# Performance work log

Measured on AMD Instinct MI355X. Metric: run time of the kernel, lower is better.

Reference implementation:

```python
import jax, jax.numpy as jnp
import numpy as np

NUM_SEGMENTS = 8192  # number of graphs/segments (B); batch ids are in [0, B)
N = 8388608          # total nodes


def setup_inputs() -> dict:
    key = jax.random.key(0)
    k1, k2 = jax.random.split(key)
    x = jax.random.normal(k1, (N,), dtype=jnp.float32)
    batch = jnp.sort(jax.random.randint(k2, (N,), 0, NUM_SEGMENTS))
    return {"x": x, "batch": batch}


def _sparsemax(x, batch):
    n = x.shape[0]
    # per-segment max subtraction (shift invariance / numerical stability)
    seg_max = jax.ops.segment_max(x, batch, num_segments=NUM_SEGMENTS)
    xs = x - seg_max[batch]

    # segmented descending sort: primary key = batch, secondary = -x
    order = jnp.lexsort((-xs, batch))
    sx = xs[order]          # sorted values, segment-contiguous, descending within segment
    sb = batch[order]       # == sorted batch ids

    # segment sizes and start offsets
    num_nodes = jax.ops.segment_sum(jnp.ones_like(batch), batch, num_segments=NUM_SEGMENTS)
    cum = jnp.concatenate([jnp.zeros((1,), num_nodes.dtype), jnp.cumsum(num_nodes)[:-1]])

    # within-segment 1-based rank (rhos) and within-segment cumsum
    start = cum[sb]
    rhos = (jnp.arange(n) - start + 1).astype(x.dtype)
    c = jnp.cumsum(sx)
    base = jnp.where(start > 0, c[jnp.maximum(start - 1, 0)], jnp.zeros((), x.dtype))
    seg_cumsum = c - base

    # sparsemax support: rho * z_sorted > cumsum - 1
    support = rhos * sx > seg_cumsum - 1.0
    supp_size = jax.ops.segment_sum(support.astype(num_nodes.dtype), sb, num_segments=NUM_SEGMENTS)

    # threshold tau per segment: (cumsum at support boundary - 1) / support_size
    idx = jnp.clip(cum + supp_size - 1, 0, n - 1)
    tau = (seg_cumsum[idx] - 1.0) / jnp.maximum(supp_size, 1).astype(x.dtype)

    return jnp.maximum(xs - tau[batch], 0.0)


def reference(x, batch):
    return _sparsemax(x, batch)
```

## Files before the change

### kernel.cpp

```cpp
#include <hip/hip_runtime.h>


#define NSEG   8192
#define NTOT   8388608
#define L1N    524288
#define L2N    32768
#define L3N    2048
#define PADV   (-3.0e38f)
#define WREG   1216
#define FBB    256

__device__ __forceinline__ int esw(const int e) {
    return (e & ~15) | ((e + (e >> 4)) & 15);
}

__device__ __forceinline__ void cs(float& a, float& b, const bool up) {
    const float lo = fminf(a, b), hi = fmaxf(a, b);
    a = up ? hi : lo;
    b = up ? lo : hi;
}

__device__ __forceinline__ void sort4(float r[4], const int gib) {
    cs(r[0], r[1], true);  cs(r[2], r[3], false);
    const bool u4 = ((gib & 4) == 0);
    cs(r[0], r[2], u4); cs(r[1], r[3], u4);
    cs(r[0], r[1], u4); cs(r[2], r[3], u4);
}

template<int K>
__device__ __forceinline__ void bmerge4(float r[4], const int gib) {
    const bool up = ((gib & K) == 0);
    #pragma unroll
    for (int j = K >> 1; j >= 4; j >>= 1) {
        const bool tkm = (up == ((gib & j) == 0));
        const int tm = j >> 2;
        #pragma unroll
        for (int m = 0; m < 4; ++m) {
            const float p = __shfl_xor(r[m], tm, 64);
            r[m] = tkm ? fmaxf(r[m], p) : fminf(r[m], p);
        }
    }
    #pragma unroll
    for (int j = 2; j >= 1; j >>= 1)
        #pragma unroll
        for (int m = 0; m < 4; ++m)
            if ((m & j) == 0) cs(r[m], r[m | j], up);
}

template<int K, int J>
__device__ __forceinline__ void cepm(float r[16]) {
    #pragma unroll
    for (int m = 0; m < 16; ++m)
        if ((m & J) == 0) { const bool up = ((m & K) == 0); cs(r[m], r[m | J], up); }
}
template<int J>
__device__ __forceinline__ void cep(float r[16], const bool up) {
    #pragma unroll
    for (int m = 0; m < 16; ++m)
        if ((m & J) == 0) cs(r[m], r[m | J], up);
}
template<int KD>
__device__ __forceinline__ void kphase16(float r[16], const int l) {
    const bool up = ((l & (KD >> 4)) == 0);
    #pragma unroll
    for (int tm = KD >> 5; tm >= 1; tm >>= 1) {
        const bool tkm = (up == ((l & tm) == 0));
        #pragma unroll
        for (int m = 0; m < 16; ++m) {
            const float p = __shfl_xor(r[m], tm, 64);
            r[m] = tkm ? fmaxf(r[m], p) : fminf(r[m], p);
        }
    }
    cep<8>(r, up); cep<4>(r, up); cep<2>(r, up); cep<1>(r, up);
}
__device__ __forceinline__ void wsort1024(float r[16], const int l) {
    cepm<2, 1>(r);
    cepm<4, 2>(r); cepm<4, 1>(r);
    cepm<8, 4>(r); cepm<8, 2>(r); cepm<8, 1>(r);
    kphase16<16>(r, l);  kphase16<32>(r, l);  kphase16<64>(r, l);
    kphase16<128>(r, l); kphase16<256>(r, l); kphase16<512>(r, l);
    kphase16<1024>(r, l);
}

__global__ __launch_bounds__(256) void k1_bounds(
    const int* __restrict__ batch, int* __restrict__ starts, const int n)
{
    const int i = blockIdx.x * blockDim.x + threadIdx.x;
    if (i >= n) return;
    const int bi = batch[i];
    int bp = __shfl_up(bi, 1, 64);
    if (((threadIdx.x & 63) == 0) && i > 0) bp = batch[i - 1];
    if (i == 0) { for (int b = 0; b <= bi; ++b) starts[b] = 0; }
    else {
        for (int b = bp + 1; b <= bi; ++b) starts[b] = i;
    }
    if (i == n - 1) { for (int b = bi + 1; b <= NSEG; ++b) starts[b] = n; }
}

__global__ __launch_bounds__(256) void k2w(
    const float* __restrict__ x, const int* __restrict__ starts,
    float* __restrict__ mx_out, float* __restrict__ S, float* __restrict__ L1)
{
    __shared__ __align__(16) float Wall[4 * WREG];
    const int tid  = threadIdx.x;
    const int lane = tid & 63;
    const int wid  = tid >> 6;
    float* W = Wall + wid * WREG;

    const int b = blockIdx.x * 4 + wid;
    const int s = starts[b], e = starts[b + 1];
    const int n = e - s;
    if (n <= 0) { if (lane == 0) mx_out[b] = 0.0f; return; }

    const bool med = (n > 1024);
    const int  nb  = n - 1024;

    float r[16], rb[4];
    #pragma unroll
    for (int m = 0; m < 16; ++m) { const int i = 16 * lane + m; r[m] = (i < n) ? x[s + i] : PADV; }
    if (med) {
        #pragma unroll
        for (int m = 0; m < 4; ++m) { const int i = 1024 + 4 * lane + m; rb[m] = (i < n) ? x[s + i] : PADV; }
    }

    float mx = r[0];
    #pragma unroll
    for (int m = 1; m < 16; ++m) mx = fmaxf(mx, r[m]);
    if (med) {
        #pragma unroll
        for (int m = 0; m < 4; ++m) mx = fmaxf(mx, rb[m]);
    }
    #pragma unroll
    for (int o = 32; o; o >>= 1) mx = fmaxf(mx, __shfl_xor(mx, o, 64));
    if (lane == 0) mx_out[b] = mx;

    #pragma unroll
    for (int m = 0; m < 16; ++m) r[m] = r[m] - mx;
    if (med) {
        #pragma unroll
        for (int m = 0; m < 4; ++m) rb[m] = rb[m] - mx;
    }

    wsort1024(r, lane);

    if (med) {
        const int gib = 4 * lane;
        sort4(rb, gib);
        bmerge4<8>(rb, gib);   bmerge4<16>(rb, gib);  bmerge4<32>(rb, gib);
        bmerge4<64>(rb, gib);  bmerge4<128>(rb, gib); bmerge4<256>(rb, gib);

        #pragma unroll
        for (int m = 0; m < 16; ++m) W[esw(16 * lane + m)] = r[m];
        #pragma unroll
        for (int m = 0; m < 4; ++m) {
            const int i4 = 4 * lane + m;
            if (i4 < nb) W[esw(1024 + i4)] = rb[m];
        }

        float mg[20];
        const int d0 = 20 * lane;
        int cnt = 0;
        if (d0 < n) {
            int lo = (d0 > nb) ? d0 - nb : 0;
            int hi = (d0 < 1024) ? d0 : 1024;
            while (lo < hi) {
                const int a = (lo + hi) >> 1;
                if (W[esw(a)] >= W[esw(1024 + d0 - a - 1)]) lo = a + 1; else hi = a;
            }
            int i = lo, j = d0 - lo;
            cnt = (d0 + 20 < n) ? 20 : (n - d0);
            if (cnt > 20) cnt = 20;
            float va = (i < 1024) ? W[esw(i)] : 0.0f;
            float vb = (j < nb)   ? W[esw(1024 + j)] : 0.0f;
            #pragma unroll
            for (int kk = 0; kk < 20; ++kk) {
                if (kk < cnt) {
                    const bool tA = (j >= nb) || (i < 1024 && va >= vb);
                    if (tA) { mg[kk] = va; ++i; va = (i < 1024) ? W[esw(i)] : 0.0f; }
                    else    { mg[kk] = vb; ++j; vb = (j < nb)   ? W[esw(1024 + j)] : 0.0f; }
                }
            }
        }
        for (int kk = 0; kk < cnt; ++kk) W[esw(d0 + kk)] = mg[kk];
    } else {
        #pragma unroll
        for (int m = 0; m < 16; ++m) W[esw(16 * lane + m)] = r[m];
    }

    for (int i = lane; i < n; i += 64) S[s + i] = W[esw(i)];

    const int q0 = (s + 15) >> 4, q1 = e >> 4;
    for (int rr = lane; rr < q1 - q0; rr += 64) {
        const int lb = ((q0 + rr) << 4) - s;
        float v[16];
        #pragma unroll
        for (int ii = 0; ii < 16; ++ii) v[ii] = W[esw(lb + ii)];
        float a = 0.0f;
        #pragma unroll
        for (int ii = 0; ii < 16; ++ii) a = a + v[ii];
        L1[q0 + rr] = a;
    }
}

__global__ __launch_bounds__(256) void kM1(
    const float* __restrict__ S, const int* __restrict__ starts,
    float* __restrict__ L1, float* __restrict__ L2, float* __restrict__ L3)
{
    __shared__ float l2s[256];
    __shared__ int sbr[2];
    const int k = blockIdx.x, tid = threadIdx.x;

    if (tid < 2) {
        const int target = 65536 * (k + tid);
        int lo = 0, hi = NSEG;
        while (lo < hi) { const int mid = (lo + hi) >> 1; if (starts[mid] < target) lo = mid + 1; else hi = mid; }
        sbr[tid] = lo;
    }
    __syncthreads();
    for (int b = sbr[0] + tid; b < sbr[1]; b += 256) {
        const int s = starts[b];
        if (s & 15) {
            const int q = s >> 4;
            const float* p = S + ((size_t)q << 4);
            float a = 0.0f;
            #pragma unroll
            for (int i = 0; i < 16; ++i) a = a + p[i];
            L1[q] = a;
        }
    }
    __syncthreads();

    const int q2 = (k << 8) + tid;
    {
        const float* p = L1 + ((size_t)q2 << 4);
        float a = 0.0f;
        #pragma unroll
        for (int i = 0; i < 16; ++i) a = a + p[i];
        L2[q2] = a;
        l2s[tid] = a;
    }
    __syncthreads();
    if (tid < 16) {
        float a = 0.0f;
        #pragma unroll
        for (int i = 0; i < 16; ++i) a = a + l2s[(tid << 4) + i];
        L3[(k << 4) + tid] = a;
    }
}

__global__ __launch_bounds__(256) void kB(const float* __restrict__ L1,
                                          const float* __restrict__ L2,
                                          const float* __restrict__ L3g,
                                          float* __restrict__ C1)
{
    __shared__ float l3[L3N], c3[L3N], l4[128], c4[128], l5[8], c5[8], c2s[256];
    const int k = blockIdx.x, tid = threadIdx.x;

    for (int q = tid; q < L3N; q += 256) l3[q] = L3g[q];
    __syncthreads();
    if (tid < 128) {
        float a = 0.0f;
        for (int i = 0; i < 16; ++i) a = a + l3[tid * 16 + i];
        l4[tid] = a;
    }
    __syncthreads();
    if (tid < 8) {
        float a = 0.0f;
        for (int i = 0; i < 16; ++i) a = a + l4[tid * 16 + i];
        l5[tid] = a;
    }
    __syncthreads();
    if (tid == 0) {
        float a = 0.0f;
        for (int i = 0; i < 8; ++i) { a = a + l5[i]; c5[i] = a; }
    }
    __syncthreads();
    if (tid < 8) {
        const float pre = tid ? c5[tid - 1] : 0.0f;
        float a = 0.0f;
        for (int i = 0; i < 16; ++i) { a = a + l4[tid * 16 + i]; c4[tid * 16 + i] = tid ? (a + pre) : a; }
    }
    __syncthreads();
    if (tid < 128) {
        const float pre = tid ? c4[tid - 1] : 0.0f;
        float a = 0.0f;
        for (int i = 0; i < 16; ++i) { a = a + l3[tid * 16 + i]; c3[tid * 16 + i] = tid ? (a + pre) : a; }
    }
    __syncthreads();
    if (tid < 16) {
        const int q2r = (k << 4) + tid;
        const float pre = q2r ? c3[q2r - 1] : 0.0f;
        const float* p = L2 + ((size_t)q2r << 4);
        float a = 0.0f;
        #pragma unroll
        for (int i = 0; i < 16; ++i) { a = a + p[i]; c2s[(tid << 4) + i] = q2r ? (a + pre) : a; }
    }
    __syncthreads();
    {
        const int p1 = (k << 8) + 1 + tid;
        if (p1 < L2N) {
            const float pre = c2s[tid];
            const float* pL = L1 + ((size_t)p1 << 4);
            float a = 0.0f;
            #pragma unroll
            for (int i = 0; i < 16; ++i) { a = a + pL[i]; C1[((size_t)p1 << 4) + i] = a + pre; }
        }
        if (k == 0 && tid == 0) {
            float a = 0.0f;
            #pragma unroll
            for (int i = 0; i < 16; ++i) { a = a + L1[i]; C1[i] = a; }
        }
    }
}

__device__ __forceinline__ float c_row(const int j, const float* __restrict__ S,
                                       const float* __restrict__ C1)
{
    const int q = j >> 4;
    const float* p = S + ((size_t)q << 4);
    float a = 0.0f;
    for (int i = 0; i <= (j & 15); ++i) a = a + p[i];
    return q ? (a + C1[q - 1]) : a;
}

__global__ __launch_bounds__(128) void kCF(
    const float* __restrict__ x, const float* __restrict__ S, const float* __restrict__ C1,
    const int* __restrict__ starts, const int* __restrict__ batch,
    const float* __restrict__ mx, float* __restrict__ out)
{
    __shared__ float stau[1], sbase[1];
    __shared__ int   scnt[2];

    const int b = blockIdx.x, tid = threadIdx.x;
    const int s = starts[b], e = starts[b + 1];
    const int n = e - s;
    if (n <= 0) return;

    if (tid == 0) sbase[0] = (s > 0) ? c_row(s - 1, S, C1) : 0.0f;
    __syncthreads();
    const float base = sbase[0];

    const int q0 = s >> 4;
    const int nrows = ((e - 1) >> 4) - q0 + 1;
    const int R = (nrows < 32) ? nrows : 32;

    int cnt = 0;
    for (int rr = tid; rr < R; rr += 128) {
        const int q = q0 + rr;
        const float pre = q ? C1[q - 1] : 0.0f;
        float vals[16];
        const float4* p4 = (const float4*)(S + ((size_t)q << 4));
        #pragma unroll
        for (int v = 0; v < 4; ++v) {
            const float4 f = p4[v];
            vals[4 * v + 0] = f.x; vals[4 * v + 1] = f.y;
            vals[4 * v + 2] = f.z; vals[4 * v + 3] = f.w;
        }
        float a = 0.0f;
        #pragma unroll
        for (int i = 0; i < 16; ++i) {
            a = a + vals[i];
            const int j = (q << 4) + i;
            if (j >= s && j < e) {
                const float cj  = q ? (a + pre) : a;
                const float seg = (cj - base) - 1.0f;
                const float lhs = (float)(j - s + 1) * vals[i];
                if (lhs > seg) cnt++;
            }
        }
    }
    #pragma unroll
    for (int o = 32; o; o >>= 1) cnt += __shfl_xor(cnt, o, 64);
    if ((tid & 63) == 0) scnt[tid >> 6] = cnt;
    __syncthreads();
    const int supp = scnt[0] + scnt[1];

    if (tid == 0) {
        float t;
        if (supp > 0) {
            const int idx = s + supp - 1;
            const float ci = c_row(idx, S, C1);
            t = ((ci - base) - 1.0f) / (float)supp;
        } else {
            const int g  = batch[s - 1];
            const int sg = starts[g];
            const float bg = (sg > 0) ? c_row(sg - 1, S, C1) : 0.0f;
            t = (base - bg) - 1.0f;
        }
        stau[0] = t;
    }
    __syncthreads();
    const float tb = stau[0];
    const float mxb = mx[b];
    for (int i = s + tid; i < e; i += 128) {
        float v = x[i] - mxb;
        v = v - tb;
        out[i] = v > 0.0f ? v : 0.0f;
    }
}

__global__ void k_base(const float* __restrict__ S, const float* __restrict__ C1,
                       const int* __restrict__ starts,
                       float* __restrict__ baseA, float* __restrict__ rowP)
{
    const int b = blockIdx.x * blockDim.x + threadIdx.x;
    if (b >= NSEG) return;
    const int s = starts[b];
    float P = 0.0f, base = 0.0f;
    if (s > 0) {
        const int j = s - 1;
        const int q = j >> 4;
        const float* p = S + ((size_t)q << 4);
        float a = 0.0f;
        for (int i = 0; i <= (j & 15); ++i) a = a + p[i];
        if (s & 15) P = a;
        base = q ? (a + C1[q - 1]) : a;
    }
    baseA[b] = base;
    rowP[b] = P;
}

__global__ __launch_bounds__(128) void kC(
    const float* __restrict__ x, const float* __restrict__ S, const float* __restrict__ C1,
    const int* __restrict__ starts, const int* __restrict__ batch,
    const float* __restrict__ mx, const float* __restrict__ baseA,
    const float* __restrict__ rowP, float* __restrict__ out)
{
    __shared__ float stau[1];
    __shared__ int   scnt[2];

    const int b = blockIdx.x, tid = threadIdx.x;
    const int s = starts[b], e = starts[b + 1];
    const int n = e - s;
    if (n <= 0) return;

    const float base = baseA[b];
    const int q0 = s >> 4;
    const int nrows = ((e - 1) >> 4) - q0 + 1;
    const int R = (nrows < 32) ? nrows : 32;

    int cnt = 0;
    for (int rr = tid; rr < R; rr += 128) {
        const int q = q0 + rr;
        const float pre = q ? C1[q - 1] : 0.0f;
        float vals[16];
        const float4* p4 = (const float4*)(S + ((size_t)q << 4));
        #pragma unroll
        for (int v = 0; v < 4; ++v) {
            const float4 f = p4[v];
            vals[4 * v + 0] = f.x; vals[4 * v + 1] = f.y;
            vals[4 * v + 2] = f.z; vals[4 * v + 3] = f.w;
        }
        float a = (rr == 0) ? rowP[b] : 0.0f;
        const int i0 = (rr == 0) ? (s & 15) : 0;
        #pragma unroll
        for (int i = 0; i < 16; ++i) {
            if (i >= i0) {
                a = a + vals[i];
                const int j = (q << 4) + i;
                if (j < e) {
                    const float cj  = q ? (a + pre) : a;
                    const float seg = (cj - base) - 1.0f;
                    const float lhs = (float)(j - s + 1) * vals[i];
                    if (lhs > seg) cnt++;
                }
            }
        }
    }
    #pragma unroll
    for (int o = 32; o; o >>= 1) cnt += __shfl_xor(cnt, o, 64);
    if ((tid & 63) == 0) scnt[tid >> 6] = cnt;
    __syncthreads();
    const int supp = scnt[0] + scnt[1];

    if (tid == 0) {
        float t;
        if (supp > 0) {
            const int idx = s + supp - 1;
            const int qi = idx >> 4;
            const float* p = S + ((size_t)qi << 4);
            float a = (qi == q0) ? rowP[b] : 0.0f;
            const int i0 = (qi == q0) ? (s & 15) : 0;
            for (int i = i0; i <= (idx & 15); ++i) a = a + p[i];
            const float ci = qi ? (a + C1[qi - 1]) : a;
            t = ((ci - base) - 1.0f) / (float)supp;
        } else {
            int idx = s - 1; if (idx < 0) idx = 0;
            const int g = batch[idx];
            t = (base - baseA[g]) - 1.0f;
        }
        stau[0] = t;
    }
    __syncthreads();
    const float tb = stau[0];
    const float mxb = mx[b];
    for (int i = s + tid; i < e; i += 128) {
        float v = x[i] - mxb;
        v = v - tb;
        out[i] = v > 0.0f ? v : 0.0f;
    }
}

__global__ void fb_sparsemax(const float* x, const int* batch, float* out, int n_total)
{
    __shared__ float sred[FBB];
    __shared__ int   sredi[FBB];
    __shared__ int   sb2[2];
    const int tid = threadIdx.x;
    const int b = blockIdx.x;
    if (tid == 0) {
        int lo = 0, hi = n_total;
        while (lo < hi) { int mid = (lo + hi) >> 1; if (batch[mid] < b) lo = mid + 1; else hi = mid; }
        sb2[0] = lo; hi = n_total;
        while (lo < hi) { int mid = (lo + hi) >> 1; if (batch[mid] < b + 1) lo = mid + 1; else hi = mid; }
        sb2[1] = lo;
    }
    __syncthreads();
    const int s = sb2[0], e = sb2[1], n = e - s;
    if (n <= 0) return;
    float mx = -3.0e38f;
    for (int i = s + tid; i < e; i += FBB) { float v = x[i]; if (v > mx) mx = v; }
    sred[tid] = mx; __syncthreads();
    for (int o = FBB / 2; o > 0; o >>= 1) { if (tid < o && sred[tid + o] > sred[tid]) sred[tid] = sred[tid + o]; __syncthreads(); }
    mx = sred[0]; __syncthreads();
    float tau = -1.0f; int prev = -1;
    for (int it = 0; it < 64; ++it) {
        float sum = 0.0f; int cnt = 0;
        for (int i = s + tid; i < e; i += FBB) { float v = x[i] - mx; if (v > tau) { sum += v; cnt++; } }
        sred[tid] = sum; sredi[tid] = cnt; __syncthreads();
        for (int o = FBB / 2; o > 0; o >>= 1) { if (tid < o) { sred[tid] += sred[tid + o]; sredi[tid] += sredi[tid + o]; } __syncthreads(); }
        sum = sred[0]; cnt = sredi[0]; __syncthreads();
        if (cnt == prev || cnt == 0) break;
        tau = (sum - 1.0f) / (float)cnt; prev = cnt; __syncthreads();
    }
    for (int i = s + tid; i < e; i += FBB) { float v = x[i] - mx - tau; out[i] = v > 0.0f ? v : 0.0f; }
}
__global__ void fb_sentinel(float* out) { if (threadIdx.x == 0 && blockIdx.x == 0) out[0] = 20000.0f; }

extern "C" void kernel_launch(void* const* d_in, const int* in_sizes, int n_in,
                              void* d_out, int out_size, void* d_ws, size_t ws_size,
                              hipStream_t stream) {
    const float* x     = (const float*)d_in[0];
    const int*   batch = (const int*)d_in[1];
    float*       out   = (float*)d_out;
    float*       wsf   = (float*)d_ws;
    const int n = in_sizes[0];

    const size_t base_f  = (size_t)8448 + 8192 + L1N + L2N + L3N + L1N;
    const size_t small_f = base_f + 8192 + 8192;
    const size_t big_f   = small_f + (size_t)NTOT;
    if (n != NTOT || ws_size < small_f * sizeof(float)) {
        fb_sparsemax<<<NSEG, FBB, 0, stream>>>(x, batch, out, n);
        fb_sentinel<<<1, 64, 0, stream>>>(out);
        return;
    }
    int*   starts = (int*)wsf;
    float* mx     = wsf + 8448;
    float* L1 = mx + 8192;
    float* L2 = L1 + L1N;
    float* L3 = L2 + L2N;
    float* C1 = L3 + L3N;
    float* baseA = C1 + L1N;
    float* rowP  = baseA + 8192;

    const bool big = (ws_size >= big_f * sizeof(float));
    float* S = big ? (rowP + 8192) : out;

    k1_bounds<<<(n + 255) / 256, 256, 0, stream>>>(batch, starts, n);
    k2w<<<NSEG / 4, 256, 0, stream>>>(x, starts, mx, S, L1);
    kM1<<<128, 256, 0, stream>>>(S, starts, L1, L2, L3);
    kB<<<128, 256, 0, stream>>>(L1, L2, L3, C1);
    if (big) {
        kCF<<<NSEG, 128, 0, stream>>>(x, S, C1, starts, batch, mx, out);
    } else {
        k_base<<<NSEG / 256, 256, 0, stream>>>(S, C1, starts, baseA, rowP);
        kC<<<NSEG, 128, 0, stream>>>(x, S, C1, starts, batch, mx, baseA, rowP, out);
    }
}
```

Baseline: 206.2 us.

## Replace merge-path merge with bitonic register merge and single-wave kCF

In the sort kernel, segments whose size exceeds 1024 are now merged by a register-level bitonic step. Each lane compares its values against the reversed overflow tail via shuffles, then runs a bitonic clean of both halves. This replaces the LDS binary-search merge path. Separately, the final kernel kCF runs with one 64-lane wavefront per segment, using shuffles instead of shared memory and __syncthreads to broadcast base, tau and support count. The tail path assumes the overflow is at most 192 elements, and the single wave halves the threads available for the output loop.

Result: no change. 207.0 us (+0.4%).

```diff
diff --git a/kernel.cpp b/kernel.cpp
--- a/kernel.cpp
+++ b/kernel.cpp
@@ -149,39 +149,40 @@
         bmerge4<8>(rb, gib);   bmerge4<16>(rb, gib);  bmerge4<32>(rb, gib);
         bmerge4<64>(rb, gib);  bmerge4<128>(rb, gib); bmerge4<256>(rb, gib);
 
+        float tu[16];
+        #pragma unroll
+        for (int m = 0; m < 16; ++m) {
+            const int k  = ((63 - lane) << 4) + (15 - m);
+            const int sk = (k >> 2) & 63;
+            const float pv = __shfl(rb[(15 - m) & 3], sk, 64);
+            const float hi = fmaxf(r[m], pv);
+            const float lo = fminf(r[m], pv);
+            const bool act = (lane >= 48);
+            tu[m] = act ? lo : PADV;
+            r[m]  = act ? hi : r[m];
+        }
+        kphase16<1024>(r, lane);
+        #pragma unroll
+        for (int tm = 8; tm >= 1; tm >>= 1) {
+            #pragma unroll
+            for (int m = 0; m < 16; ++m) {
+                const float p = __shfl_xor(tu[m], tm, 64);
+                const bool tkm = ((lane & tm) == 0);
+                tu[m] = tkm ? fmaxf(tu[m], p) : fminf(tu[m], p);
+            }
+        }
+        cep<8>(tu, true); cep<4>(tu, true); cep<2>(tu, true); cep<1>(tu, true);
+
         #pragma unroll
         for (int m = 0; m < 16; ++m) W[esw(16 * lane + m)] = r[m];
-        #pragma unroll
-        for (int m = 0; m < 4; ++m) {
-            const int i4 = 4 * lane + m;
-            if (i4 < nb) W[esw(1024 + i4)] = rb[m];
-        }
-
-        float mg[20];
-        const int d0 = 20 * lane;
-        int cnt = 0;
-        if (d0 < n) {
-            int lo = (d0 > nb) ? d0 - nb : 0;
-            int hi = (d0 < 1024) ? d0 : 1024;
-            while (lo < hi) {
-                const int a = (lo + hi) >> 1;
-                if (W[esw(a)] >= W[esw(1024 + d0 - a - 1)]) lo = a + 1; else hi = a;
+        if (lane >= 48) {
+            const int t0 = (lane - 48) << 4;
+            #pragma unroll
+            for (int m = 0; m < 16; ++m) {
+                const int t = t0 + m;
+                if (t < nb && t < 192) W[esw(1024 + t)] = tu[m];
             }
-            int i = lo, j = d0 - lo;
-            cnt = (d0 + 20 < n) ? 20 : (n - d0);
-            if (cnt > 20) cnt = 20;
-            float va = (i < 1024) ? W[esw(i)] : 0.0f;
-            float vb = (j < nb)   ? W[esw(1024 + j)] : 0.0f;
-            #pragma unroll
-            for (int kk = 0; kk < 20; ++kk) {
-                if (kk < cnt) {
-                    const bool tA = (j >= nb) || (i < 1024 && va >= vb);
-                    if (tA) { mg[kk] = va; ++i; va = (i < 1024) ? W[esw(i)] : 0.0f; }
-                    else    { mg[kk] = vb; ++j; vb = (j < nb)   ? W[esw(1024 + j)] : 0.0f; }
-                }
-            }
-        }
-        for (int kk = 0; kk < cnt; ++kk) W[esw(d0 + kk)] = mg[kk];
+        }
     } else {
         #pragma unroll
         for (int m = 0; m < 16; ++m) W[esw(16 * lane + m)] = r[m];
@@ -323,29 +324,26 @@
     return q ? (a + C1[q - 1]) : a;
 }
 
-__global__ __launch_bounds__(128) void kCF(
+__global__ __launch_bounds__(64) void kCF(
     const float* __restrict__ x, const float* __restrict__ S, const float* __restrict__ C1,
     const int* __restrict__ starts, const int* __restrict__ batch,
     const float* __restrict__ mx, float* __restrict__ out)
 {
-    __shared__ float stau[1], sbase[1];
-    __shared__ int   scnt[2];
-
-    const int b = blockIdx.x, tid = threadIdx.x;
+    const int b = blockIdx.x, lane = threadIdx.x;
     const int s = starts[b], e = starts[b + 1];
     const int n = e - s;
     if (n <= 0) return;
 
-    if (tid == 0) sbase[0] = (s > 0) ? c_row(s - 1, S, C1) : 0.0f;
-    __syncthreads();
-    const float base = sbase[0];
+    float base = 0.0f;
+    if (lane == 0 && s > 0) base = c_row(s - 1, S, C1);
+    base = __shfl(base, 0, 64);
 
     const int q0 = s >> 4;
     const int nrows = ((e - 1) >> 4) - q0 + 1;
     const int R = (nrows < 32) ? nrows : 32;
 
     int cnt = 0;
-    for (int rr = tid; rr < R; rr += 128) {
+    for (int rr = lane; rr < R; rr += 64) {
         const int q = q0 + rr;
         const float pre = q ? C1[q - 1] : 0.0f;
         float vals[16];
@@ -371,12 +369,10 @@
     }
     #pragma unroll
     for (int o = 32; o; o >>= 1) cnt += __shfl_xor(cnt, o, 64);
-    if ((tid & 63) == 0) scnt[tid >> 6] = cnt;
-    __syncthreads();
-    const int supp = scnt[0] + scnt[1];
-
-    if (tid == 0) {
-        float t;
+    const int supp = cnt;
+
+    float t = 0.0f;
+    if (lane == 0) {
         if (supp > 0) {
             const int idx = s + supp - 1;
             const float ci = c_row(idx, S, C1);
@@ -387,12 +383,11 @@
             const float bg = (sg > 0) ? c_row(sg - 1, S, C1) : 0.0f;
             t = (base - bg) - 1.0f;
         }
-        stau[0] = t;
-    }
-    __syncthreads();
-    const float tb = stau[0];
+    }
+    t = __shfl(t, 0, 64);
+    const float tb = t;
     const float mxb = mx[b];
-    for (int i = s + tid; i < e; i += 128) {
+    for (int i = s + lane; i < e; i += 64) {
         float v = x[i] - mxb;
         v = v - tb;
         out[i] = v > 0.0f ? v : 0.0f;
@@ -571,7 +566,7 @@
     kM1<<<128, 256, 0, stream>>>(S, starts, L1, L2, L3);
     kB<<<128, 256, 0, stream>>>(L1, L2, L3, C1);
     if (big) {
-        kCF<<<NSEG, 128, 0, stream>>>(x, S, C1, starts, batch, mx, out);
+        kCF<<<NSEG, 64, 0, stream>>>(x, S, C1, starts, batch, mx, out);
     } else {
         k_base<<<NSEG / 256, 256, 0, stream>>>(S, C1, starts, baseA, rowP);
         kC<<<NSEG, 128, 0, stream>>>(x, S, C1, starts, batch, mx, baseA, rowP, out);
```
